# Performance work log

Measured on AMD Instinct MI355X. Metric: run time of the kernel, lower is better.

## Reference

```python
import jax, jax.numpy as jnp
import numpy as np
from jax import lax

B, P, N, D, L, H = 16, 8192, 1024, 384, 12, 6
HD = D // H
K_NEI = 5          # HomogeneityLoss k
KL_RATIO = 1.0


def setup_inputs() -> dict:
    key = jax.random.key(0)
    ks = jax.random.split(key, 10)
    s = lambda i, shape, sc=0.02: (jax.random.normal(ks[i], shape, jnp.float32) * sc)
    return dict(
        pts=jax.random.normal(ks[0], (B, P, 3), jnp.float32),
        grid=jax.random.normal(ks[1], (B, N, 3), jnp.float32),
        embed_w=s(2, (3, D), 0.1),
        proj_w=s(3, (D, 3), 0.1),
        ln1_w=jnp.ones((L, D)), ln1_b=jnp.zeros((L, D)),
        qkv_w=s(4, (L, D, 3 * D)), qkv_b=jnp.zeros((L, 3 * D)),
        attn_w=s(5, (L, D, D)), attn_b=jnp.zeros((L, D)),
        ln2_w=jnp.ones((L, D)), ln2_b=jnp.zeros((L, D)),
        mlp_w1=s(6, (L, D, 4 * D)), mlp_b1=jnp.zeros((L, 4 * D)),
        mlp_w2=s(7, (L, 4 * D, D)), mlp_b2=jnp.zeros((L, D)),
    )


def _ln(x, w, b):
    m = jnp.mean(x, -1, keepdims=True)
    v = jnp.var(x, -1, keepdims=True)
    return (x - m) * lax.rsqrt(v + 1e-5) * w + b


def _transformer(x, params):
    def layer(x, p):
        l1w, l1b, qw, qb, aw, ab, l2w, l2b, m1w, m1b, m2w, m2b = p
        h = _ln(x, l1w, l1b)
        qkv = h @ qw + qb                                   # [B,N,3D]
        q, k, v = jnp.split(qkv, 3, axis=-1)
        rs = lambda t: t.reshape(B, N, H, HD).transpose(0, 2, 1, 3)  # [B,H,N,HD]
        q, k, v = rs(q), rs(k), rs(v)
        att = jax.nn.softmax(jnp.einsum('bhnd,bhmd->bhnm', q, k) / np.sqrt(HD), axis=-1)
        o = jnp.einsum('bhnm,bhmd->bhnd', att, v).transpose(0, 2, 1, 3).reshape(B, N, D)
        x = x + (o @ aw + ab)
        h = _ln(x, l2w, l2b)
        x = x + (jax.nn.gelu(h @ m1w + m1b) @ m2w + m2b)
        return x, None
    x, _ = lax.scan(layer, x, params)
    return x


def _fps(points):  # points: [P,3] -> N int32 indices (farthest point sampling)
    def body(carry, _):
        dists, last = carry
        d = jnp.sum((points - points[last]) ** 2, axis=-1)
        dists = jnp.minimum(dists, d)
        return (dists, jnp.argmax(dists).astype(jnp.int32)), last
    init = (jnp.full((points.shape[0],), 1e10, points.dtype), jnp.int32(0))
    (_, _), idxs = lax.scan(body, init, None, length=N)
    return idxs


def reference(pts, grid, embed_w, proj_w, ln1_w, ln1_b, qkv_w, qkv_b,
              attn_w, attn_b, ln2_w, ln2_b, mlp_w1, mlp_b1, mlp_w2, mlp_b2):
    params = (ln1_w, ln1_b, qkv_w, qkv_b, attn_w, attn_b,
              ln2_w, ln2_b, mlp_w1, mlp_b1, mlp_w2, mlp_b2)
    x = grid @ embed_w                                      # [B,N,D]
    x = _transformer(x, params)
    pred = x @ proj_w                                       # [B,N,3]

    # FPS centers from the raw point cloud
    idxs = jax.vmap(_fps)(pts)                              # [B,N]
    centers = jnp.take_along_axis(pts, idxs[..., None], axis=1)  # [B,N,3]

    # Chamfer L1 (symmetric mean of nearest-neighbor L2 norms)
    d = jnp.linalg.norm(pred[:, :, None, :] - centers[:, None, :, :], axis=-1)  # [B,N,N]
    rec = 0.5 * (d.min(axis=2).mean(axis=1) + d.min(axis=1).mean(axis=1))       # [B]

    # Homogeneity: mean dist of K_NEI nearest neighbors -> softmax -> KL(q||p)
    dd = jnp.linalg.norm(pred[:, :, None, :] - pred[:, None, :, :], axis=-1)    # [B,N,N]
    neg_vals, _ = lax.top_k(-dd, K_NEI + 1)                 # smallest K+1 dists
    mean_d = (-neg_vals[..., 1:]).mean(axis=-1)             # drop self -> [B,N]
    logp = jax.nn.log_softmax(mean_d, axis=-1)
    q = 1.0 / N
    kl = jnp.sum(q * (jnp.log(q) - logp), axis=-1)          # [B]

    return rec.mean(), KL_RATIO * kl.mean()
```

## Files before the change

kernel.cpp:

```cpp
#include <hip/hip_runtime.h>
#include <math.h>

#define B_   16
#define P_   8192
#define N_   1024
#define D_   384
#define L_   12
#define H_   6
#define HD_  64
#define M_   (B_*N_)
#define DQKV_ (3*D_)
#define DH_   (4*D_)

typedef unsigned short ushort_t;
typedef __attribute__((ext_vector_type(8))) short short8;
typedef __attribute__((ext_vector_type(4))) float floatx4;

__device__ __forceinline__ ushort_t f2bf(float f) {
    unsigned u = __float_as_uint(f);
    unsigned rounding = 0x7fffu + ((u >> 16) & 1u);
    return (ushort_t)((u + rounding) >> 16);
}
__device__ __forceinline__ float bf2f(ushort_t u) {
    return __uint_as_float(((unsigned)u) << 16);
}

__global__ __launch_bounds__(D_) void embed_kernel(const float* __restrict__ g,
                                                   const float* __restrict__ ew,
                                                   float* __restrict__ X) {
    int m = blockIdx.x;
    int d = threadIdx.x;
    float g0 = g[m*3+0], g1 = g[m*3+1], g2 = g[m*3+2];
    X[(size_t)m*D_ + d] = g0*ew[0*D_+d] + g1*ew[1*D_+d] + g2*ew[2*D_+d];
}

__global__ __launch_bounds__(256) void transcast_kernel(const float* __restrict__ W,
                                                        ushort_t* __restrict__ Wt,
                                                        int K, int Nc) {
    __shared__ float t[32][33];
    const float* Wl = W + (size_t)blockIdx.z*K*Nc;
    ushort_t* Wtl = Wt + (size_t)blockIdx.z*K*Nc;
    int n0 = blockIdx.x*32, k0 = blockIdx.y*32;
    int tx = threadIdx.x & 31, ty = threadIdx.x >> 5;
#pragma unroll
    for (int j = 0; j < 32; j += 8)
        t[ty+j][tx] = Wl[(size_t)(k0+ty+j)*Nc + n0+tx];
    __syncthreads();
#pragma unroll
    for (int j = 0; j < 32; j += 8)
        Wtl[(size_t)(n0+ty+j)*K + k0+tx] = f2bf(t[tx][ty+j]);
}

__global__ __launch_bounds__(256) void ln_kernel(const float* __restrict__ Xin,
                                                 const float* __restrict__ w,
                                                 const float* __restrict__ bvec,
                                                 ushort_t* __restrict__ out) {
    int wid = threadIdx.x >> 6, lane = threadIdx.x & 63;
    int row = blockIdx.x*4 + wid;
    const float* xr = Xin + (size_t)row*D_;
    float v[6];
#pragma unroll
    for (int i = 0; i < 6; i++) v[i] = xr[lane + i*64];
    float s = 0.f;
#pragma unroll
    for (int i = 0; i < 6; i++) s += v[i];
#pragma unroll
    for (int off = 32; off; off >>= 1) s += __shfl_xor(s, off, 64);
    float mean = s * (1.0f/(float)D_);
    float vs = 0.f;
#pragma unroll
    for (int i = 0; i < 6; i++) { float d = v[i]-mean; vs += d*d; }
#pragma unroll
    for (int off = 32; off; off >>= 1) vs += __shfl_xor(vs, off, 64);
    float var = vs * (1.0f/(float)D_);
    float rstd = 1.0f / sqrtf(var + 1e-5f);
    ushort_t* orow = out + (size_t)row*D_;
#pragma unroll
    for (int i = 0; i < 6; i++) {
        int e = lane + i*64;
        orow[e] = f2bf((v[i]-mean)*rstd*w[e] + bvec[e]);
    }
}

__device__ __forceinline__ float gelu_f(float x) {
    const float c = 0.7978845608028654f;
    float x3 = x*x*x;
    return 0.5f*x*(1.0f + tanhf(c*(x + 0.044715f*x3)));
}

template<int EPI>
__global__ __launch_bounds__(256) void mfma_gemm(const ushort_t* __restrict__ A,
                                                 const ushort_t* __restrict__ Wt,
                                                 const float* __restrict__ bias,
                                                 void* __restrict__ Cout,
                                                 ushort_t* __restrict__ VT,
                                                 int K, int Nc) {
    __shared__ __attribute__((aligned(16))) ushort_t smem[2*128*32];
    ushort_t* smA = smem;
    ushort_t* smB = smem + 128*32;
    int tid = threadIdx.x;
    int lane = tid & 63, w = tid >> 6;
    int wm = w >> 1, wn = w & 1;
    int L = lane & 15, G = lane >> 4;
    int rowBase = blockIdx.y * 128, colBase = blockIdx.x * 128;

    floatx4 acc[4][4];
#pragma unroll
    for (int i = 0; i < 4; i++)
#pragma unroll
        for (int j = 0; j < 4; j++) acc[i][j] = (floatx4){0.f,0.f,0.f,0.f};

    int sr = tid >> 2;
    int kc = tid & 3;
    const ushort_t* Ag = A  + (size_t)(rowBase + sr)*K + kc*8;
    const ushort_t* Bg = Wt + (size_t)(colBase + sr)*K + kc*8;
    size_t step64 = (size_t)64*K;

    short8 ra0, ra1, rb0, rb1;
    ra0 = *(const short8*)(Ag);
    ra1 = *(const short8*)(Ag + step64);
    rb0 = *(const short8*)(Bg);
    rb1 = *(const short8*)(Bg + step64);

    for (int k0 = 0; k0 < K; k0 += 32) {
        __syncthreads();
        *(short8*)(smA + sr*32 + kc*8)        = ra0;
        *(short8*)(smA + (64+sr)*32 + kc*8)   = ra1;
        *(short8*)(smB + sr*32 + kc*8)        = rb0;
        *(short8*)(smB + (64+sr)*32 + kc*8)   = rb1;
        __syncthreads();
        if (k0 + 32 < K) {
            ra0 = *(const short8*)(Ag + k0 + 32);
            ra1 = *(const short8*)(Ag + step64 + k0 + 32);
            rb0 = *(const short8*)(Bg + k0 + 32);
            rb1 = *(const short8*)(Bg + step64 + k0 + 32);
        }
        short8 af[4], bfr[4];
#pragma unroll
        for (int t = 0; t < 4; t++) {
            af[t]  = *(const short8*)(smA + (wm*64 + t*16 + L)*32 + G*8);
            bfr[t] = *(const short8*)(smB + (wn*64 + t*16 + L)*32 + G*8);
        }
#pragma unroll
        for (int mt = 0; mt < 4; mt++)
#pragma unroll
            for (int nt = 0; nt < 4; nt++)
                acc[mt][nt] = __builtin_amdgcn_mfma_f32_16x16x32_bf16(
                    af[mt], bfr[nt], acc[mt][nt], 0, 0, 0);
        __syncthreads();
    }

    __syncthreads();

    if (EPI == 3 && colBase >= 2*D_) {
        int cBase = colBase + wn*64 + L;
        int rBase = rowBase + wm*64 + G*4;
#pragma unroll
        for (int nt = 0; nt < 4; nt++) {
            int col = cBase + nt*16;
            float bv = bias[col];
            int hh = (col - 2*D_) >> 6, d = (col - 2*D_) & 63;
#pragma unroll
            for (int mt = 0; mt < 4; mt++) {
#pragma unroll
                for (int r = 0; r < 4; r++) {
                    int row = rBase + mt*16 + r;
                    int b = row >> 10, n = row & 1023;
                    VT[(((size_t)b*H_ + hh)*64 + d)*N_ + n] = f2bf(acc[mt][nt][r] + bv);
                }
            }
        }
    } else if (EPI == 1) {
        float* fs = (float*)smem + w*1024;
        int orow = lane >> 2, c4 = lane & 3;
#pragma unroll
        for (int mt = 0; mt < 4; mt++) {
#pragma unroll
            for (int nt = 0; nt < 4; nt++) {
                float bv = bias[colBase + wn*64 + nt*16 + L];
#pragma unroll
                for (int r = 0; r < 4; r++)
                    fs[(G*4+r)*64 + nt*16 + L] = acc[mt][nt][r] + bv;
            }
            float* og = (float*)Cout + (size_t)(rowBase + wm*64 + mt*16 + orow)*Nc
                        + colBase + wn*64;
#pragma unroll
            for (int kk = 0; kk < 4; kk++) {
                float4 sv = *(float4*)(fs + orow*64 + kk*16 + c4*4);
                float4 gv = *(float4*)(og + kk*16 + c4*4);
                gv.x += sv.x; gv.y += sv.y; gv.z += sv.z; gv.w += sv.w;
                *(float4*)(og + kk*16 + c4*4) = gv;
            }
        }
    } else {
        ushort_t* us = smem + w*1152;
        int orow = lane >> 2, oc = lane & 3;
#pragma unroll
        for (int mt = 0; mt < 4; mt++) {
#pragma unroll
            for (int nt = 0; nt < 4; nt++) {
                float bv = bias[colBase + wn*64 + nt*16 + L];
#pragma unroll
                for (int r = 0; r < 4; r++) {
                    float v = acc[mt][nt][r] + bv;
                    if (EPI == 2) v = gelu_f(v);
                    us[(G*4+r)*72 + nt*16 + L] = f2bf(v);
                }
            }
            short8 o0 = *(short8*)(us + orow*72 + oc*8);
            short8 o1 = *(short8*)(us + orow*72 + 32 + oc*8);
            ushort_t* og = (ushort_t*)Cout + (size_t)(rowBase + wm*64 + mt*16 + orow)*Nc
                           + colBase + wn*64;
            *(short8*)(og + oc*8) = o0;
            *(short8*)(og + 32 + oc*8) = o1;
        }
    }
}

#define LPAD 72
__global__ __launch_bounds__(256) void fattn_kernel(const ushort_t* __restrict__ QKV,
                                                    const ushort_t* __restrict__ VT,
                                                    ushort_t* __restrict__ O) {
    __shared__ __attribute__((aligned(16))) ushort_t Ks[64*LPAD];
    __shared__ __attribute__((aligned(16))) ushort_t Vs[64*LPAD];
    __shared__ __attribute__((aligned(16))) ushort_t Pw[4*16*LPAD];
    int b = blockIdx.z, h = blockIdx.y;
    int qBase = blockIdx.x * 64;
    int tid = threadIdx.x;
    int lane = tid & 63, w = tid >> 6;
    int L = lane & 15, G = lane >> 4;

    short8 qf[2];
    {
        const ushort_t* qp = QKV + ((size_t)(b*N_ + qBase + w*16 + L))*DQKV_ + h*HD_ + G*8;
        qf[0] = *(const short8*)(qp);
        qf[1] = *(const short8*)(qp + 32);
    }

    floatx4 oacc[4];
#pragma unroll
    for (int nt = 0; nt < 4; nt++) oacc[nt] = (floatx4){0.f,0.f,0.f,0.f};
    float mrow[4], lrow[4];
#pragma unroll
    for (int r = 0; r < 4; r++) { mrow[r] = -3.0e38f; lrow[r] = 0.f; }

    ushort_t* pw = Pw + w*16*LPAD;
    const ushort_t* Kbase = QKV + (size_t)b*N_*DQKV_ + D_ + h*HD_;
    const ushort_t* Vbase = VT + ((size_t)b*H_ + h)*64*N_;

    int srow = tid >> 3;
    int dc   = tid & 7;
    const ushort_t* Kg0 = Kbase + (size_t)srow*DQKV_ + dc*8;
    const ushort_t* Kg1 = Kbase + (size_t)(srow+32)*DQKV_ + dc*8;
    const ushort_t* Vg0 = Vbase + (size_t)srow*N_ + dc*8;
    const ushort_t* Vg1 = Vbase + (size_t)(srow+32)*N_ + dc*8;

    short8 rk0, rk1, rv0, rv1;
    rk0 = *(const short8*)(Kg0);
    rk1 = *(const short8*)(Kg1);
    rv0 = *(const short8*)(Vg0);
    rv1 = *(const short8*)(Vg1);

    for (int kt = 0; kt < N_/64; kt++) {
        __syncthreads();
        *(short8*)(Ks + srow*LPAD + dc*8)       = rk0;
        *(short8*)(Ks + (srow+32)*LPAD + dc*8)  = rk1;
        *(short8*)(Vs + srow*LPAD + dc*8)       = rv0;
        *(short8*)(Vs + (srow+32)*LPAD + dc*8)  = rv1;
        __syncthreads();
        if (kt + 1 < N_/64) {
            rk0 = *(const short8*)(Kg0 + (size_t)(kt+1)*64*DQKV_);
            rk1 = *(const short8*)(Kg1 + (size_t)(kt+1)*64*DQKV_);
            rv0 = *(const short8*)(Vg0 + (kt+1)*64);
            rv1 = *(const short8*)(Vg1 + (kt+1)*64);
        }

        floatx4 sc[4];
#pragma unroll
        for (int ct = 0; ct < 4; ct++) sc[ct] = (floatx4){0.f,0.f,0.f,0.f};
#pragma unroll
        for (int ks = 0; ks < 2; ks++)
#pragma unroll
            for (int ct = 0; ct < 4; ct++) {
                short8 bf = *(const short8*)(Ks + (ct*16 + L)*LPAD + ks*32 + G*8);
                sc[ct] = __builtin_amdgcn_mfma_f32_16x16x32_bf16(qf[ks], bf, sc[ct], 0, 0, 0);
            }

        float rmax[4], rsum[4];
#pragma unroll
        for (int r = 0; r < 4; r++) {
#pragma unroll
            for (int ct = 0; ct < 4; ct++) sc[ct][r] *= 0.125f;
            rmax[r] = fmaxf(fmaxf(sc[0][r], sc[1][r]), fmaxf(sc[2][r], sc[3][r]));
        }
#pragma unroll
        for (int off = 1; off < 16; off <<= 1)
#pragma unroll
            for (int r = 0; r < 4; r++) rmax[r] = fmaxf(rmax[r], __shfl_xor(rmax[r], off, 64));
        float corr[4];
#pragma unroll
        for (int r = 0; r < 4; r++) {
            float mn = fmaxf(mrow[r], rmax[r]);
            corr[r] = __expf(mrow[r] - mn);
            mrow[r] = mn;
            rsum[r] = 0.f;
#pragma unroll
            for (int ct = 0; ct < 4; ct++) {
                float p = __expf(sc[ct][r] - mn);
                sc[ct][r] = p;
                rsum[r] += p;
            }
        }
#pragma unroll
        for (int off = 1; off < 16; off <<= 1)
#pragma unroll
            for (int r = 0; r < 4; r++) rsum[r] += __shfl_xor(rsum[r], off, 64);
#pragma unroll
        for (int r = 0; r < 4; r++) lrow[r] = lrow[r]*corr[r] + rsum[r];

#pragma unroll
        for (int ct = 0; ct < 4; ct++)
#pragma unroll
            for (int r = 0; r < 4; r++)
                pw[(G*4 + r)*LPAD + ct*16 + L] = f2bf(sc[ct][r]);
#pragma unroll
        for (int nt = 0; nt < 4; nt++)
#pragma unroll
            for (int r = 0; r < 4; r++) oacc[nt][r] *= corr[r];

#pragma unroll
        for (int ks = 0; ks < 2; ks++) {
            short8 pf = *(const short8*)(pw + L*LPAD + ks*32 + G*8);
#pragma unroll
            for (int nt = 0; nt < 4; nt++) {
                short8 vf = *(const short8*)(Vs + (nt*16 + L)*LPAD + ks*32 + G*8);
                oacc[nt] = __builtin_amdgcn_mfma_f32_16x16x32_bf16(pf, vf, oacc[nt], 0, 0, 0);
            }
        }
    }

    float inv[4];
#pragma unroll
    for (int r = 0; r < 4; r++) inv[r] = 1.0f / lrow[r];
#pragma unroll
    for (int nt = 0; nt < 4; nt++)
#pragma unroll
        for (int r = 0; r < 4; r++)
            pw[(G*4 + r)*LPAD + nt*16 + L] = f2bf(oacc[nt][r]*inv[r]);
    int orow = lane >> 2, oc = lane & 3;
    short8 o0 = *(short8*)(pw + orow*LPAD + oc*8);
    short8 o1 = *(short8*)(pw + orow*LPAD + 32 + oc*8);
    ushort_t* og = O + (size_t)(b*N_ + qBase + w*16 + orow)*D_ + h*HD_;
    *(short8*)(og + oc*8) = o0;
    *(short8*)(og + 32 + oc*8) = o1;
}

__global__ __launch_bounds__(256) void proj_kernel(const float* __restrict__ X,
                                                   const float* __restrict__ pw,
                                                   float* __restrict__ pred) {
    int m = blockIdx.x*256 + threadIdx.x;
    const float* xr = X + (size_t)m*D_;
    float a0 = 0.f, a1 = 0.f, a2 = 0.f;
    for (int k = 0; k < D_; k++) {
        float xv = xr[k];
        a0 += xv*pw[k*3+0]; a1 += xv*pw[k*3+1]; a2 += xv*pw[k*3+2];
    }
    pred[m*3+0] = a0; pred[m*3+1] = a1; pred[m*3+2] = a2;
}

__global__ __launch_bounds__(1024) void fps_kernel(const float* __restrict__ pts,
                                                   float* __restrict__ centers) {
    __shared__ float Lx[P_], Ly[P_], Lz[P_];
    __shared__ unsigned long long slot[2][16];
    int b = blockIdx.x, t = threadIdx.x;
    const float* pb = pts + (size_t)b*P_*3;
    float px[8], py[8], pz[8], dist[8];
#pragma unroll
    for (int j = 0; j < 8; j++) {
        int p = j*1024 + t;
        px[j] = pb[p*3+0]; py[j] = pb[p*3+1]; pz[j] = pb[p*3+2];
        Lx[p] = px[j]; Ly[p] = py[j]; Lz[p] = pz[j];
        dist[j] = 1e10f;
    }
    int wid = t >> 6;
    int winner = 0;
    __syncthreads();
    for (int it = 0; it < N_; it++) {
        float lx = Lx[winner], ly = Ly[winner], lz = Lz[winner];
        if (t == 0) {
            float* c = centers + ((size_t)b*N_ + it)*3;
            c[0] = lx; c[1] = ly; c[2] = lz;
        }
        unsigned long long best = 0ull;
#pragma unroll
        for (int j = 0; j < 8; j++) {
            float dx = __fsub_rn(px[j], lx);
            float dy = __fsub_rn(py[j], ly);
            float dz = __fsub_rn(pz[j], lz);
            float d = __fadd_rn(__fadd_rn(__fmul_rn(dx,dx), __fmul_rn(dy,dy)), __fmul_rn(dz,dz));
            d = fminf(dist[j], d);
            dist[j] = d;
            unsigned long long pk = ((unsigned long long)__float_as_uint(d) << 32)
                                  | (unsigned)(~(unsigned)(j*1024 + t));
            best = (pk > best) ? pk : best;
        }
#pragma unroll
        for (int off = 32; off; off >>= 1) {
            unsigned long long o = __shfl_xor(best, off, 64);
            best = (o > best) ? o : best;
        }
        int par = it & 1;
        if ((t & 63) == 0) slot[par][wid] = best;
        __syncthreads();
        unsigned long long s0, s1, s2, s3, s4, s5, s6, s7;
        s0 = slot[par][0];  s1 = slot[par][1];  s2 = slot[par][2];  s3 = slot[par][3];
        s4 = slot[par][4];  s5 = slot[par][5];  s6 = slot[par][6];  s7 = slot[par][7];
        s0 = (s1 > s0) ? s1 : s0;  s2 = (s3 > s2) ? s3 : s2;
        s4 = (s5 > s4) ? s5 : s4;  s6 = (s7 > s6) ? s7 : s6;
        s0 = (s2 > s0) ? s2 : s0;  s4 = (s6 > s4) ? s6 : s4;
        s0 = (s4 > s0) ? s4 : s0;
        unsigned long long u0, u1, u2, u3, u4, u5, u6, u7;
        u0 = slot[par][8];  u1 = slot[par][9];  u2 = slot[par][10]; u3 = slot[par][11];
        u4 = slot[par][12]; u5 = slot[par][13]; u6 = slot[par][14]; u7 = slot[par][15];
        u0 = (u1 > u0) ? u1 : u0;  u2 = (u3 > u2) ? u3 : u2;
        u4 = (u5 > u4) ? u5 : u4;  u6 = (u7 > u6) ? u7 : u6;
        u0 = (u2 > u0) ? u2 : u0;  u4 = (u6 > u4) ? u6 : u4;
        u0 = (u4 > u0) ? u4 : u0;
        s0 = (u0 > s0) ? u0 : s0;
        winner = (int)(~(unsigned)(s0 & 0xFFFFFFFFull));
    }
}

__global__ __launch_bounds__(256) void nnmin_kernel(const float* __restrict__ Asrc,
                                                    const float* __restrict__ Bsrc,
                                                    float* __restrict__ outmin) {
    int b = blockIdx.y;
    int i = blockIdx.x*256 + threadIdx.x;
    __shared__ float tile[256][3];
    const float* ar = Asrc + ((size_t)b*N_ + i)*3;
    float ax = ar[0], ay = ar[1], az = ar[2];
    float best = 3.0e38f;
    for (int j0 = 0; j0 < N_; j0 += 256) {
        __syncthreads();
        const float* br = Bsrc + ((size_t)b*N_ + j0 + threadIdx.x)*3;
        tile[threadIdx.x][0] = br[0]; tile[threadIdx.x][1] = br[1]; tile[threadIdx.x][2] = br[2];
        __syncthreads();
        for (int j = 0; j < 256; j++) {
            float dx = ax - tile[j][0], dy = ay - tile[j][1], dz = az - tile[j][2];
            float d = dx*dx + dy*dy + dz*dz;
            best = fminf(best, d);
        }
    }
    outmin[(size_t)b*N_ + i] = sqrtf(best);
}

__global__ __launch_bounds__(256) void knn_kernel(const float* __restrict__ Pp,
                                                  float* __restrict__ mean_d) {
    int b = blockIdx.y;
    int i = blockIdx.x*256 + threadIdx.x;
    __shared__ float tile[256][3];
    const float* ar = Pp + ((size_t)b*N_ + i)*3;
    float ax = ar[0], ay = ar[1], az = ar[2];
    float s[6];
#pragma unroll
    for (int q = 0; q < 6; q++) s[q] = 3.0e38f;
    for (int j0 = 0; j0 < N_; j0 += 256) {
        __syncthreads();
        const float* br = Pp + ((size_t)b*N_ + j0 + threadIdx.x)*3;
        tile[threadIdx.x][0] = br[0]; tile[threadIdx.x][1] = br[1]; tile[threadIdx.x][2] = br[2];
        __syncthreads();
        for (int j = 0; j < 256; j++) {
            float dx = ax - tile[j][0], dy = ay - tile[j][1], dz = az - tile[j][2];
            float d = dx*dx + dy*dy + dz*dz;
            if (d < s[5]) {
                s[5] = d;
#pragma unroll
                for (int q = 5; q > 0; q--)
                    if (s[q] < s[q-1]) { float tmp = s[q]; s[q] = s[q-1]; s[q-1] = tmp; }
            }
        }
    }
    float msum = sqrtf(s[1]) + sqrtf(s[2]) + sqrtf(s[3]) + sqrtf(s[4]) + sqrtf(s[5]);
    mean_d[(size_t)b*N_ + i] = msum * 0.2f;
}

__global__ __launch_bounds__(256) void kl_kernel(const float* __restrict__ md,
                                                 float* __restrict__ klb) {
    int b = blockIdx.x, t = threadIdx.x;
    const float* row = md + (size_t)b*N_;
    float v[4];
#pragma unroll
    for (int i = 0; i < 4; i++) v[i] = row[t + i*256];
    float mx = fmaxf(fmaxf(v[0], v[1]), fmaxf(v[2], v[3]));
#pragma unroll
    for (int off = 32; off; off >>= 1) mx = fmaxf(mx, __shfl_xor(mx, off, 64));
    __shared__ float redm[4], rse[4], rsx[4];
    int wid = t >> 6, lane = t & 63;
    if (lane == 0) redm[wid] = mx;
    __syncthreads();
    mx = fmaxf(fmaxf(redm[0], redm[1]), fmaxf(redm[2], redm[3]));
    float se = 0.f, sx = 0.f;
#pragma unroll
    for (int i = 0; i < 4; i++) { se += expf(v[i]-mx); sx += v[i]; }
#pragma unroll
    for (int off = 32; off; off >>= 1) { se += __shfl_xor(se, off, 64); sx += __shfl_xor(sx, off, 64); }
    if (lane == 0) { rse[wid] = se; rsx[wid] = sx; }
    __syncthreads();
    if (t == 0) {
        float SE = rse[0]+rse[1]+rse[2]+rse[3];
        float SX = rsx[0]+rsx[1]+rsx[2]+rsx[3];
        klb[b] = mx + logf(SE) - SX*(1.0f/(float)N_) - logf((float)N_);
    }
}

__global__ __launch_bounds__(256) void final_kernel(const float* __restrict__ rma,
                                                    const float* __restrict__ rmb,
                                                    const float* __restrict__ klb,
                                                    float* __restrict__ out) {
    int t = threadIdx.x;
    float s = 0.f;
    for (int i = t; i < B_*N_; i += 256) s += rma[i] + rmb[i];
#pragma unroll
    for (int off = 32; off; off >>= 1) s += __shfl_xor(s, off, 64);
    __shared__ float red[4];
    int wid = t >> 6, lane = t & 63;
    if (lane == 0) red[wid] = s;
    __syncthreads();
    if (t == 0) {
        float S = red[0]+red[1]+red[2]+red[3];
        out[0] = 0.5f*S/(float)(B_*N_);
        float K = 0.f;
        for (int b = 0; b < B_; b++) K += klb[b];
        out[1] = K/(float)B_;
    }
}

extern "C" void kernel_launch(void* const* d_in, const int* in_sizes, int n_in,
                              void* d_out, int out_size, void* d_ws, size_t ws_size,
                              hipStream_t stream) {
    (void)in_sizes; (void)n_in; (void)out_size; (void)ws_size;
    const float* pts     = (const float*)d_in[0];
    const float* grid    = (const float*)d_in[1];
    const float* embed_w = (const float*)d_in[2];
    const float* proj_w  = (const float*)d_in[3];
    const float* ln1_w   = (const float*)d_in[4];
    const float* ln1_b   = (const float*)d_in[5];
    const float* qkv_w   = (const float*)d_in[6];
    const float* qkv_b   = (const float*)d_in[7];
    const float* attn_w  = (const float*)d_in[8];
    const float* attn_b  = (const float*)d_in[9];
    const float* ln2_w   = (const float*)d_in[10];
    const float* ln2_b   = (const float*)d_in[11];
    const float* mlp_w1  = (const float*)d_in[12];
    const float* mlp_b1  = (const float*)d_in[13];
    const float* mlp_w2  = (const float*)d_in[14];
    const float* mlp_b2  = (const float*)d_in[15];
    float* out = (float*)d_out;

    float*    X     = (float*)d_ws;
    ushort_t* Hb16  = (ushort_t*)(X + (size_t)M_*D_);
    ushort_t* BIG16 = Hb16 + (size_t)M_*D_;
    ushort_t* VT    = BIG16 + (size_t)M_*DH_;
    ushort_t* WQ    = VT  + (size_t)B_*H_*HD_*N_;
    ushort_t* WA    = WQ  + (size_t)L_*DQKV_*D_;
    ushort_t* WM1   = WA  + (size_t)L_*D_*D_;
    ushort_t* WM2   = WM1 + (size_t)L_*DH_*D_;
    float*    PRED  = (float*)(WM2 + (size_t)L_*D_*DH_);
    float*    CENT  = PRED + (size_t)M_*3;
    float*    RMA   = CENT + (size_t)B_*N_*3;
    float*    RMB   = RMA  + (size_t)B_*N_;
    float*    MEAND = RMB  + (size_t)B_*N_;
    float*    KLB   = MEAND + (size_t)B_*N_;

    transcast_kernel<<<dim3(DQKV_/32, D_/32,  L_), 256, 0, stream>>>(qkv_w,  WQ,  D_,  DQKV_);
    transcast_kernel<<<dim3(D_/32,    D_/32,  L_), 256, 0, stream>>>(attn_w, WA,  D_,  D_);
    transcast_kernel<<<dim3(DH_/32,   D_/32,  L_), 256, 0, stream>>>(mlp_w1, WM1, D_,  DH_);
    transcast_kernel<<<dim3(D_/32,    DH_/32, L_), 256, 0, stream>>>(mlp_w2, WM2, DH_, D_);

    fps_kernel<<<B_, 1024, 0, stream>>>(pts, CENT);

    embed_kernel<<<M_, D_, 0, stream>>>(grid, embed_w, X);

    for (int l = 0; l < L_; l++) {
        ln_kernel<<<M_/4, 256, 0, stream>>>(X, ln1_w + l*D_, ln1_b + l*D_, Hb16);
        mfma_gemm<3><<<dim3(DQKV_/128, M_/128), 256, 0, stream>>>(
            Hb16, WQ + (size_t)l*DQKV_*D_, qkv_b + l*DQKV_, BIG16, VT, D_, DQKV_);
        fattn_kernel<<<dim3(N_/64, H_, B_), 256, 0, stream>>>(BIG16, VT, Hb16);
        mfma_gemm<1><<<dim3(D_/128, M_/128), 256, 0, stream>>>(
            Hb16, WA + (size_t)l*D_*D_, attn_b + l*D_, X, nullptr, D_, D_);
        ln_kernel<<<M_/4, 256, 0, stream>>>(X, ln2_w + l*D_, ln2_b + l*D_, Hb16);
        mfma_gemm<2><<<dim3(DH_/128, M_/128), 256, 0, stream>>>(
            Hb16, WM1 + (size_t)l*DH_*D_, mlp_b1 + l*DH_, BIG16, nullptr, D_, DH_);
        mfma_gemm<1><<<dim3(D_/128, M_/128), 256, 0, stream>>>(
            BIG16, WM2 + (size_t)l*D_*DH_, mlp_b2 + l*D_, X, nullptr, DH_, D_);
    }

    proj_kernel<<<M_/256, 256, 0, stream>>>(X, proj_w, PRED);

    nnmin_kernel<<<dim3(N_/256, B_), 256, 0, stream>>>(PRED, CENT, RMA);
    nnmin_kernel<<<dim3(N_/256, B_), 256, 0, stream>>>(CENT, PRED, RMB);
    knn_kernel<<<dim3(N_/256, B_), 256, 0, stream>>>(PRED, MEAND);
    kl_kernel<<<B_, 256, 0, stream>>>(MEAND, KLB);
    final_kernel<<<1, 256, 0, stream>>>(RMA, RMB, KLB, out);
}
```

Measured before the change: 4.847 ms.

## Pad GEMM LDS, widen attention KV tiles, remap blocks, rework FPS and projection

```diff
diff --git a/kernel.cpp b/kernel.cpp
--- a/kernel.cpp
+++ b/kernel.cpp
@@ -13,6 +13,7 @@
 #define DH_   (4*D_)
 
 typedef unsigned short ushort_t;
+typedef unsigned long long u64_t;
 typedef __attribute__((ext_vector_type(8))) short short8;
 typedef __attribute__((ext_vector_type(4))) float floatx4;
 
@@ -88,6 +89,7 @@
     return 0.5f*x*(1.0f + tanhf(c*(x + 0.044715f*x3)));
 }
 
+#define GS_ 34
 template<int EPI>
 __global__ __launch_bounds__(256) void mfma_gemm(const ushort_t* __restrict__ A,
                                                  const ushort_t* __restrict__ Wt,
@@ -95,9 +97,9 @@
                                                  void* __restrict__ Cout,
                                                  ushort_t* __restrict__ VT,
                                                  int K, int Nc) {
-    __shared__ __attribute__((aligned(16))) ushort_t smem[2*128*32];
+    __shared__ __attribute__((aligned(16))) ushort_t smem[2*128*GS_];
     ushort_t* smA = smem;
-    ushort_t* smB = smem + 128*32;
+    ushort_t* smB = smem + 128*GS_;
     int tid = threadIdx.x;
     int lane = tid & 63, w = tid >> 6;
     int wm = w >> 1, wn = w & 1;
@@ -124,10 +126,10 @@
 
     for (int k0 = 0; k0 < K; k0 += 32) {
         __syncthreads();
-        *(short8*)(smA + sr*32 + kc*8)        = ra0;
-        *(short8*)(smA + (64+sr)*32 + kc*8)   = ra1;
-        *(short8*)(smB + sr*32 + kc*8)        = rb0;
-        *(short8*)(smB + (64+sr)*32 + kc*8)   = rb1;
+        *(short8*)(smA + sr*GS_ + kc*8)        = ra0;
+        *(short8*)(smA + (64+sr)*GS_ + kc*8)   = ra1;
+        *(short8*)(smB + sr*GS_ + kc*8)        = rb0;
+        *(short8*)(smB + (64+sr)*GS_ + kc*8)   = rb1;
         __syncthreads();
         if (k0 + 32 < K) {
             ra0 = *(const short8*)(Ag + k0 + 32);
@@ -138,8 +140,8 @@
         short8 af[4], bfr[4];
 #pragma unroll
         for (int t = 0; t < 4; t++) {
-            af[t]  = *(const short8*)(smA + (wm*64 + t*16 + L)*32 + G*8);
-            bfr[t] = *(const short8*)(smB + (wn*64 + t*16 + L)*32 + G*8);
+            af[t]  = *(const short8*)(smA + (wm*64 + t*16 + L)*GS_ + G*8);
+            bfr[t] = *(const short8*)(smB + (wn*64 + t*16 + L)*GS_ + G*8);
         }
 #pragma unroll
         for (int mt = 0; mt < 4; mt++)
@@ -217,15 +219,20 @@
     }
 }
 
-#define LPAD 72
+#define KS_ 66
+#define VS_ 130
 __global__ __launch_bounds__(256) void fattn_kernel(const ushort_t* __restrict__ QKV,
                                                     const ushort_t* __restrict__ VT,
                                                     ushort_t* __restrict__ O) {
-    __shared__ __attribute__((aligned(16))) ushort_t Ks[64*LPAD];
-    __shared__ __attribute__((aligned(16))) ushort_t Vs[64*LPAD];
-    __shared__ __attribute__((aligned(16))) ushort_t Pw[4*16*LPAD];
-    int b = blockIdx.z, h = blockIdx.y;
-    int qBase = blockIdx.x * 64;
+    __shared__ __attribute__((aligned(16))) ushort_t Ks[128*KS_];
+    __shared__ __attribute__((aligned(16))) ushort_t Vs[64*VS_];
+    __shared__ __attribute__((aligned(16))) ushort_t Pw[4*16*VS_];
+    int blk = blockIdx.x;
+    int xcd = blk & 7, idx = blk >> 3;
+    int bh = xcd*12 + (idx >> 4);
+    int qb = idx & 15;
+    int b = bh / H_, h = bh % H_;
+    int qBase = qb * 64;
     int tid = threadIdx.x;
     int lane = tid & 63, w = tid >> 6;
     int L = lane & 15, G = lane >> 4;
@@ -244,54 +251,57 @@
 #pragma unroll
     for (int r = 0; r < 4; r++) { mrow[r] = -3.0e38f; lrow[r] = 0.f; }
 
-    ushort_t* pw = Pw + w*16*LPAD;
+    ushort_t* pw = Pw + w*16*VS_;
     const ushort_t* Kbase = QKV + (size_t)b*N_*DQKV_ + D_ + h*HD_;
     const ushort_t* Vbase = VT + ((size_t)b*H_ + h)*64*N_;
 
-    int srow = tid >> 3;
-    int dc   = tid & 7;
-    const ushort_t* Kg0 = Kbase + (size_t)srow*DQKV_ + dc*8;
-    const ushort_t* Kg1 = Kbase + (size_t)(srow+32)*DQKV_ + dc*8;
-    const ushort_t* Vg0 = Vbase + (size_t)srow*N_ + dc*8;
-    const ushort_t* Vg1 = Vbase + (size_t)(srow+32)*N_ + dc*8;
-
-    short8 rk0, rk1, rv0, rv1;
-    rk0 = *(const short8*)(Kg0);
-    rk1 = *(const short8*)(Kg1);
-    rv0 = *(const short8*)(Vg0);
-    rv1 = *(const short8*)(Vg1);
-
-    for (int kt = 0; kt < N_/64; kt++) {
-        __syncthreads();
-        *(short8*)(Ks + srow*LPAD + dc*8)       = rk0;
-        *(short8*)(Ks + (srow+32)*LPAD + dc*8)  = rk1;
-        *(short8*)(Vs + srow*LPAD + dc*8)       = rv0;
-        *(short8*)(Vs + (srow+32)*LPAD + dc*8)  = rv1;
-        __syncthreads();
-        if (kt + 1 < N_/64) {
-            rk0 = *(const short8*)(Kg0 + (size_t)(kt+1)*64*DQKV_);
-            rk1 = *(const short8*)(Kg1 + (size_t)(kt+1)*64*DQKV_);
-            rv0 = *(const short8*)(Vg0 + (kt+1)*64);
-            rv1 = *(const short8*)(Vg1 + (kt+1)*64);
-        }
-
-        floatx4 sc[4];
-#pragma unroll
-        for (int ct = 0; ct < 4; ct++) sc[ct] = (floatx4){0.f,0.f,0.f,0.f};
+    short8 rk[4], rv[4];
+#pragma unroll
+    for (int i = 0; i < 4; i++) {
+        int c = tid + 256*i;
+        rk[i] = *(const short8*)(Kbase + (size_t)(c>>3)*DQKV_ + (c&7)*8);
+        rv[i] = *(const short8*)(Vbase + (size_t)(c>>4)*N_ + (c&15)*8);
+    }
+
+    for (int kt = 0; kt < N_/128; kt++) {
+        __syncthreads();
+#pragma unroll
+        for (int i = 0; i < 4; i++) {
+            int c = tid + 256*i;
+            *(short8*)(Ks + (c>>3)*KS_ + (c&7)*8)  = rk[i];
+            *(short8*)(Vs + (c>>4)*VS_ + (c&15)*8) = rv[i];
+        }
+        __syncthreads();
+        if (kt + 1 < N_/128) {
+#pragma unroll
+            for (int i = 0; i < 4; i++) {
+                int c = tid + 256*i;
+                rk[i] = *(const short8*)(Kbase + (size_t)((kt+1)*128 + (c>>3))*DQKV_ + (c&7)*8);
+                rv[i] = *(const short8*)(Vbase + (size_t)(c>>4)*N_ + (kt+1)*128 + (c&15)*8);
+            }
+        }
+
+        floatx4 sc[8];
+#pragma unroll
+        for (int ct = 0; ct < 8; ct++) sc[ct] = (floatx4){0.f,0.f,0.f,0.f};
 #pragma unroll
         for (int ks = 0; ks < 2; ks++)
 #pragma unroll
-            for (int ct = 0; ct < 4; ct++) {
-                short8 bf = *(const short8*)(Ks + (ct*16 + L)*LPAD + ks*32 + G*8);
+            for (int ct = 0; ct < 8; ct++) {
+                short8 bf = *(const short8*)(Ks + (ct*16 + L)*KS_ + ks*32 + G*8);
                 sc[ct] = __builtin_amdgcn_mfma_f32_16x16x32_bf16(qf[ks], bf, sc[ct], 0, 0, 0);
             }
 
         float rmax[4], rsum[4];
 #pragma unroll
         for (int r = 0; r < 4; r++) {
-#pragma unroll
-            for (int ct = 0; ct < 4; ct++) sc[ct][r] *= 0.125f;
-            rmax[r] = fmaxf(fmaxf(sc[0][r], sc[1][r]), fmaxf(sc[2][r], sc[3][r]));
+            float mx = sc[0][r];
+#pragma unroll
+            for (int ct = 0; ct < 8; ct++) { sc[ct][r] *= 0.125f; }
+            mx = sc[0][r];
+#pragma unroll
+            for (int ct = 1; ct < 8; ct++) mx = fmaxf(mx, sc[ct][r]);
+            rmax[r] = mx;
         }
 #pragma unroll
         for (int off = 1; off < 16; off <<= 1)
@@ -305,7 +315,7 @@
             mrow[r] = mn;
             rsum[r] = 0.f;
 #pragma unroll
-            for (int ct = 0; ct < 4; ct++) {
+            for (int ct = 0; ct < 8; ct++) {
                 float p = __expf(sc[ct][r] - mn);
                 sc[ct][r] = p;
                 rsum[r] += p;
@@ -319,21 +329,21 @@
         for (int r = 0; r < 4; r++) lrow[r] = lrow[r]*corr[r] + rsum[r];
 
 #pragma unroll
-        for (int ct = 0; ct < 4; ct++)
+        for (int ct = 0; ct < 8; ct++)
 #pragma unroll
             for (int r = 0; r < 4; r++)
-                pw[(G*4 + r)*LPAD + ct*16 + L] = f2bf(sc[ct][r]);
+                pw[(G*4 + r)*VS_ + ct*16 + L] = f2bf(sc[ct][r]);
 #pragma unroll
         for (int nt = 0; nt < 4; nt++)
 #pragma unroll
             for (int r = 0; r < 4; r++) oacc[nt][r] *= corr[r];
 
 #pragma unroll
-        for (int ks = 0; ks < 2; ks++) {
-            short8 pf = *(const short8*)(pw + L*LPAD + ks*32 + G*8);
+        for (int ks = 0; ks < 4; ks++) {
+            short8 pf = *(const short8*)(pw + L*VS_ + ks*32 + G*8);
 #pragma unroll
             for (int nt = 0; nt < 4; nt++) {
-                short8 vf = *(const short8*)(Vs + (nt*16 + L)*LPAD + ks*32 + G*8);
+                short8 vf = *(const short8*)(Vs + (nt*16 + L)*VS_ + ks*32 + G*8);
                 oacc[nt] = __builtin_amdgcn_mfma_f32_16x16x32_bf16(pf, vf, oacc[nt], 0, 0, 0);
             }
         }
@@ -346,10 +356,10 @@
     for (int nt = 0; nt < 4; nt++)
 #pragma unroll
         for (int r = 0; r < 4; r++)
-            pw[(G*4 + r)*LPAD + nt*16 + L] = f2bf(oacc[nt][r]*inv[r]);
+            pw[(G*4 + r)*VS_ + nt*16 + L] = f2bf(oacc[nt][r]*inv[r]);
     int orow = lane >> 2, oc = lane & 3;
-    short8 o0 = *(short8*)(pw + orow*LPAD + oc*8);
-    short8 o1 = *(short8*)(pw + orow*LPAD + 32 + oc*8);
+    short8 o0 = *(short8*)(pw + orow*VS_ + oc*8);
+    short8 o1 = *(short8*)(pw + orow*VS_ + 32 + oc*8);
     ushort_t* og = O + (size_t)(b*N_ + qBase + w*16 + orow)*D_ + h*HD_;
     *(short8*)(og + oc*8) = o0;
     *(short8*)(og + 32 + oc*8) = o1;
@@ -358,31 +368,42 @@
 __global__ __launch_bounds__(256) void proj_kernel(const float* __restrict__ X,
                                                    const float* __restrict__ pw,
                                                    float* __restrict__ pred) {
-    int m = blockIdx.x*256 + threadIdx.x;
+    int wid = threadIdx.x >> 6, lane = threadIdx.x & 63;
+    int m = blockIdx.x*4 + wid;
     const float* xr = X + (size_t)m*D_;
     float a0 = 0.f, a1 = 0.f, a2 = 0.f;
-    for (int k = 0; k < D_; k++) {
+#pragma unroll
+    for (int i = 0; i < 6; i++) {
+        int k = lane + i*64;
         float xv = xr[k];
         a0 += xv*pw[k*3+0]; a1 += xv*pw[k*3+1]; a2 += xv*pw[k*3+2];
     }
-    pred[m*3+0] = a0; pred[m*3+1] = a1; pred[m*3+2] = a2;
-}
-
-__global__ __launch_bounds__(1024) void fps_kernel(const float* __restrict__ pts,
-                                                   float* __restrict__ centers) {
+#pragma unroll
+    for (int off = 32; off; off >>= 1) {
+        a0 += __shfl_xor(a0, off, 64);
+        a1 += __shfl_xor(a1, off, 64);
+        a2 += __shfl_xor(a2, off, 64);
+    }
+    if (lane == 0) {
+        pred[m*3+0] = a0; pred[m*3+1] = a1; pred[m*3+2] = a2;
+    }
+}
+
+__global__ __launch_bounds__(512) void fps_kernel(const float* __restrict__ pts,
+                                                  float* __restrict__ centers) {
     __shared__ float Lx[P_], Ly[P_], Lz[P_];
-    __shared__ unsigned long long slot[2][16];
+    __shared__ u64_t slot[2][8];
     int b = blockIdx.x, t = threadIdx.x;
     const float* pb = pts + (size_t)b*P_*3;
-    float px[8], py[8], pz[8], dist[8];
-#pragma unroll
-    for (int j = 0; j < 8; j++) {
-        int p = j*1024 + t;
+    float px[16], py[16], pz[16], dist[16];
+#pragma unroll
+    for (int j = 0; j < 16; j++) {
+        int p = j*512 + t;
         px[j] = pb[p*3+0]; py[j] = pb[p*3+1]; pz[j] = pb[p*3+2];
         Lx[p] = px[j]; Ly[p] = py[j]; Lz[p] = pz[j];
         dist[j] = 1e10f;
     }
-    int wid = t >> 6;
+    int wid = t >> 6, lane = t & 63;
     int winner = 0;
     __syncthreads();
     for (int it = 0; it < N_; it++) {
@@ -391,43 +412,36 @@
             float* c = centers + ((size_t)b*N_ + it)*3;
             c[0] = lx; c[1] = ly; c[2] = lz;
         }
-        unsigned long long best = 0ull;
-#pragma unroll
-        for (int j = 0; j < 8; j++) {
+        float bd = -1.0f; int bj = 0;
+#pragma unroll
+        for (int j = 0; j < 16; j++) {
             float dx = __fsub_rn(px[j], lx);
             float dy = __fsub_rn(py[j], ly);
             float dz = __fsub_rn(pz[j], lz);
             float d = __fadd_rn(__fadd_rn(__fmul_rn(dx,dx), __fmul_rn(dy,dy)), __fmul_rn(dz,dz));
             d = fminf(dist[j], d);
             dist[j] = d;
-            unsigned long long pk = ((unsigned long long)__float_as_uint(d) << 32)
-                                  | (unsigned)(~(unsigned)(j*1024 + t));
-            best = (pk > best) ? pk : best;
-        }
+            bool gt = d > bd;
+            bd = gt ? d : bd;
+            bj = gt ? j : bj;
+        }
+        u64_t best = ((u64_t)__float_as_uint(bd) << 32)
+                   | (unsigned)(~(unsigned)(bj*512 + t));
 #pragma unroll
         for (int off = 32; off; off >>= 1) {
-            unsigned long long o = __shfl_xor(best, off, 64);
+            u64_t o = __shfl_xor(best, off, 64);
             best = (o > best) ? o : best;
         }
         int par = it & 1;
-        if ((t & 63) == 0) slot[par][wid] = best;
-        __syncthreads();
-        unsigned long long s0, s1, s2, s3, s4, s5, s6, s7;
-        s0 = slot[par][0];  s1 = slot[par][1];  s2 = slot[par][2];  s3 = slot[par][3];
-        s4 = slot[par][4];  s5 = slot[par][5];  s6 = slot[par][6];  s7 = slot[par][7];
-        s0 = (s1 > s0) ? s1 : s0;  s2 = (s3 > s2) ? s3 : s2;
-        s4 = (s5 > s4) ? s5 : s4;  s6 = (s7 > s6) ? s7 : s6;
-        s0 = (s2 > s0) ? s2 : s0;  s4 = (s6 > s4) ? s6 : s4;
-        s0 = (s4 > s0) ? s4 : s0;
-        unsigned long long u0, u1, u2, u3, u4, u5, u6, u7;
-        u0 = slot[par][8];  u1 = slot[par][9];  u2 = slot[par][10]; u3 = slot[par][11];
-        u4 = slot[par][12]; u5 = slot[par][13]; u6 = slot[par][14]; u7 = slot[par][15];
-        u0 = (u1 > u0) ? u1 : u0;  u2 = (u3 > u2) ? u3 : u2;
-        u4 = (u5 > u4) ? u5 : u4;  u6 = (u7 > u6) ? u7 : u6;
-        u0 = (u2 > u0) ? u2 : u0;  u4 = (u6 > u4) ? u6 : u4;
-        u0 = (u4 > u0) ? u4 : u0;
-        s0 = (u0 > s0) ? u0 : s0;
-        winner = (int)(~(unsigned)(s0 & 0xFFFFFFFFull));
+        if (lane == 0) slot[par][wid] = best;
+        __syncthreads();
+        u64_t v = slot[par][lane & 7];
+#pragma unroll
+        for (int off = 1; off < 8; off <<= 1) {
+            u64_t o = __shfl_xor(v, off, 64);
+            v = (o > v) ? o : v;
+        }
+        winner = (int)(~(unsigned)(v & 0xFFFFFFFFull));
     }
 }
 
@@ -577,7 +591,7 @@
     transcast_kernel<<<dim3(DH_/32,   D_/32,  L_), 256, 0, stream>>>(mlp_w1, WM1, D_,  DH_);
     transcast_kernel<<<dim3(D_/32,    DH_/32, L_), 256, 0, stream>>>(mlp_w2, WM2, DH_, D_);
 
-    fps_kernel<<<B_, 1024, 0, stream>>>(pts, CENT);
+    fps_kernel<<<B_, 512, 0, stream>>>(pts, CENT);
 
     embed_kernel<<<M_, D_, 0, stream>>>(grid, embed_w, X);
 
@@ -585,7 +599,7 @@
         ln_kernel<<<M_/4, 256, 0, stream>>>(X, ln1_w + l*D_, ln1_b + l*D_, Hb16);
         mfma_gemm<3><<<dim3(DQKV_/128, M_/128), 256, 0, stream>>>(
             Hb16, WQ + (size_t)l*DQKV_*D_, qkv_b + l*DQKV_, BIG16, VT, D_, DQKV_);
-        fattn_kernel<<<dim3(N_/64, H_, B_), 256, 0, stream>>>(BIG16, VT, Hb16);
+        fattn_kernel<<<(N_/64)*H_*B_, 256, 0, stream>>>(BIG16, VT, Hb16);
         mfma_gemm<1><<<dim3(D_/128, M_/128), 256, 0, stream>>>(
             Hb16, WA + (size_t)l*D_*D_, attn_b + l*D_, X, nullptr, D_, D_);
         ln_kernel<<<M_/4, 256, 0, stream>>>(X, ln2_w + l*D_, ln2_b + l*D_, Hb16);
@@ -595,7 +609,7 @@
             BIG16, WM2 + (size_t)l*D_*DH_, mlp_b2 + l*D_, X, nullptr, DH_, D_);
     }
 
-    proj_kernel<<<M_/256, 256, 0, stream>>>(X, proj_w, PRED);
+    proj_kernel<<<M_/4, 256, 0, stream>>>(X, proj_w, PRED);
 
     nnmin_kernel<<<dim3(N_/256, B_), 256, 0, stream>>>(PRED, CENT, RMA);
     nnmin_kernel<<<dim3(N_/256, B_), 256, 0, stream>>>(CENT, PRED, RMB);
```

Result: slower. 7.591 ms (+56.6%).
